# Optimization experiments

Measured on AMD Instinct MI355X. Metric: run time of the kernel, lower is better.

Reference implementation:

```python
import jax, jax.numpy as jnp
import numpy as np

B, T, IN, OUT = 32, 2048, 1024, 256
DT = 1.0
TAU_MIN, TAU_MAX = 15.0, 25.0


def setup_inputs() -> dict:
    key = jax.random.key(0)
    k1, k2, k3 = jax.random.split(key, 3)
    inputs = jax.random.normal(k1, (B, T, IN), dtype=jnp.float32)
    bound = float(np.sqrt(1.0 / IN))
    weight = jax.random.uniform(k2, (OUT, IN), minval=-bound, maxval=bound, dtype=jnp.float32)
    bias = jnp.zeros((OUT,), dtype=jnp.float32)
    tau = jax.random.uniform(k3, (OUT,), minval=TAU_MIN, maxval=TAU_MAX, dtype=jnp.float32)
    decay = jnp.exp(-DT / tau)  # per-channel leak alpha in (0,1)
    return {"inputs": inputs, "weight": weight, "bias": bias, "decay": decay}


def reference(inputs, weight, bias, decay):
    # Dense projection: [B,T,IN] @ [IN,OUT] -> [B,T,OUT]
    current = jnp.einsum("bti,oi->bto", inputs, weight) + bias
    # Leaky integrator: u_t = alpha * u_{t-1} + (1-alpha) * x_t, u_0 = 0
    one_minus = 1.0 - decay

    def step(u, x):  # u,x: [B,OUT]
        u = decay * u + one_minus * x
        return u, u

    u0 = jnp.zeros((inputs.shape[0], weight.shape[0]), dtype=current.dtype)
    _, us = jax.lax.scan(step, u0, jnp.swapaxes(current, 0, 1))  # [T,B,OUT]
    return jnp.swapaxes(us, 0, 1)  # [B,T,OUT]
```

## Files before the change

kernel.cpp:

```cpp
#include <hip/hip_runtime.h>

#define B_   32
#define T_   2048
#define IN_  1024
#define OUT_ 256
#define M_   (B_ * T_)

#define BM 128
#define BN 256
#define BK 64
#define NSTEPS (IN_ / BK)
#define THREADS 512

#define NC 16
#define LC (T_ / NC)

typedef __attribute__((ext_vector_type(4))) float f32x4;
typedef __attribute__((ext_vector_type(8))) __bf16 bf16x8;

__device__ __forceinline__ unsigned int f2bf_pk(float a, float b) {
    unsigned int ua = __float_as_uint(a);
    unsigned int ub = __float_as_uint(b);
    ua = (ua + 0x7fffu + ((ua >> 16) & 1u)) >> 16;
    ub = (ub + 0x7fffu + ((ub >> 16) & 1u)) >> 16;
    return ua | (ub << 16);
}

__global__ __launch_bounds__(256) void convert_w(const float* __restrict__ W,
                                                 unsigned short* __restrict__ Wb) {
    const int i = blockIdx.x * 256 + threadIdx.x;
    const float4 v = ((const float4*)W)[i];
    uint2 o;
    o.x = f2bf_pk(v.x, v.y);
    o.y = f2bf_pk(v.z, v.w);
    ((uint2*)Wb)[i] = o;
}

__global__ __launch_bounds__(THREADS, 1) void gemm_mfma(
    const float* __restrict__ A, const unsigned short* __restrict__ Wb,
    const float* __restrict__ bias, float* __restrict__ C) {
    __shared__ __align__(16) unsigned short Abuf[2][BM * BK];
    __shared__ __align__(16) unsigned short Bbuf[2][BN * BK];

    const int tid  = threadIdx.x;
    const int lane = tid & 63;
    const int wid  = tid >> 6;
    const int wm   = wid >> 2;
    const int wn   = wid & 3;
    const int l15  = lane & 15;
    const int l4   = lane >> 4;
    const int bm0  = blockIdx.x * BM;

    const int gA = tid & 7;
    int rA[2], ldsA[2];
    const float* gsrcA[2];
#pragma unroll
    for (int i = 0; i < 2; ++i) {
        const int q = tid + i * THREADS;
        rA[i] = q >> 3;
        ldsA[i] = rA[i] * BK + ((gA ^ (rA[i] & 7)) << 3);
        gsrcA[i] = A + (size_t)(bm0 + rA[i]) * IN_ + gA * 8;
    }
    int ldsB[4];
    const unsigned short* gsrcB[4];
#pragma unroll
    for (int i = 0; i < 4; ++i) {
        const int q = tid + i * THREADS;
        const int r = q >> 3;
        ldsB[i] = r * BK + ((gA ^ (r & 7)) << 3);
        gsrcB[i] = Wb + (size_t)r * IN_ + gA * 8;
    }

    f32x4 acc[4][4] = {};
    float4 a0[2], a1[2];
    int4 bst[4];

#pragma unroll
    for (int i = 0; i < 2; ++i) {
        a0[i] = *(const float4*)(gsrcA[i]);
        a1[i] = *(const float4*)(gsrcA[i] + 4);
    }
#pragma unroll
    for (int i = 0; i < 4; ++i) bst[i] = *(const int4*)(gsrcB[i]);
#pragma unroll
    for (int i = 0; i < 2; ++i) {
        int4 w;
        w.x = f2bf_pk(a0[i].x, a0[i].y); w.y = f2bf_pk(a0[i].z, a0[i].w);
        w.z = f2bf_pk(a1[i].x, a1[i].y); w.w = f2bf_pk(a1[i].z, a1[i].w);
        *(int4*)&Abuf[0][ldsA[i]] = w;
    }
#pragma unroll
    for (int i = 0; i < 4; ++i) *(int4*)&Bbuf[0][ldsB[i]] = bst[i];
    __syncthreads();

    int cur = 0;
    for (int step = 0; step < NSTEPS; ++step) {
        const int nxt = step + 1;
        if (nxt < NSTEPS) {
            const int k0 = nxt * BK;
#pragma unroll
            for (int i = 0; i < 2; ++i) {
                a0[i] = *(const float4*)(gsrcA[i] + k0);
                a1[i] = *(const float4*)(gsrcA[i] + k0 + 4);
            }
#pragma unroll
            for (int i = 0; i < 4; ++i) bst[i] = *(const int4*)(gsrcB[i] + k0);
        }
#pragma unroll
        for (int ks = 0; ks < 2; ++ks) {
            bf16x8 af[4], bfv[4];
            const int kg = (ks << 2) + l4;
#pragma unroll
            for (int mi = 0; mi < 4; ++mi) {
                const int row = wm * 64 + mi * 16 + l15;
                af[mi] = *(const bf16x8*)&Abuf[cur][row * BK + ((kg ^ (row & 7)) << 3)];
            }
#pragma unroll
            for (int ni = 0; ni < 4; ++ni) {
                const int col = wn * 64 + ni * 16 + l15;
                bfv[ni] = *(const bf16x8*)&Bbuf[cur][col * BK + ((kg ^ (col & 7)) << 3)];
            }
#pragma unroll
            for (int mi = 0; mi < 4; ++mi)
#pragma unroll
                for (int ni = 0; ni < 4; ++ni)
                    acc[mi][ni] = __builtin_amdgcn_mfma_f32_16x16x32_bf16(
                        af[mi], bfv[ni], acc[mi][ni], 0, 0, 0);
        }
        if (nxt < NSTEPS) {
#pragma unroll
            for (int i = 0; i < 2; ++i) {
                int4 w;
                w.x = f2bf_pk(a0[i].x, a0[i].y); w.y = f2bf_pk(a0[i].z, a0[i].w);
                w.z = f2bf_pk(a1[i].x, a1[i].y); w.w = f2bf_pk(a1[i].z, a1[i].w);
                *(int4*)&Abuf[cur ^ 1][ldsA[i]] = w;
            }
#pragma unroll
            for (int i = 0; i < 4; ++i) *(int4*)&Bbuf[cur ^ 1][ldsB[i]] = bst[i];
        }
        __syncthreads();
        cur ^= 1;
    }

#pragma unroll
    for (int ni = 0; ni < 4; ++ni) {
        const int col = wn * 64 + ni * 16 + l15;
        const float bv = bias[col];
#pragma unroll
        for (int mi = 0; mi < 4; ++mi) {
            const int row0 = bm0 + wm * 64 + mi * 16 + (l4 << 2);
#pragma unroll
            for (int r = 0; r < 4; ++r)
                C[(size_t)(row0 + r) * OUT_ + col] = acc[mi][ni][r] + bv;
        }
    }
}

__global__ __launch_bounds__(256) void gemm_bias(const float* __restrict__ A,
                                                 const float* __restrict__ W,
                                                 const float* __restrict__ bias,
                                                 float* __restrict__ C) {
    __shared__ float As[16][64 + 4];
    __shared__ float Ws[16][64 + 4];
    const int bm = blockIdx.y * 64;
    const int bn = blockIdx.x * 64;
    const int tid = threadIdx.x;
    const int tx = tid & 15, ty = tid >> 4;
    const int lr = tid >> 2, lc = (tid & 3) << 2;
    float acc[4][4] = {};
    const float* Ap = A + (size_t)(bm + lr) * IN_ + lc;
    const float* Wp = W + (size_t)(bn + lr) * IN_ + lc;
    for (int k0 = 0; k0 < IN_; k0 += 16) {
        const float4 a = *(const float4*)(Ap + k0);
        const float4 w = *(const float4*)(Wp + k0);
        __syncthreads();
        As[lc + 0][lr] = a.x; As[lc + 1][lr] = a.y; As[lc + 2][lr] = a.z; As[lc + 3][lr] = a.w;
        Ws[lc + 0][lr] = w.x; Ws[lc + 1][lr] = w.y; Ws[lc + 2][lr] = w.z; Ws[lc + 3][lr] = w.w;
        __syncthreads();
#pragma unroll
        for (int kk = 0; kk < 16; ++kk) {
            const float4 av = *(const float4*)&As[kk][ty << 2];
            const float4 wv = *(const float4*)&Ws[kk][tx << 2];
            const float a0[4] = {av.x, av.y, av.z, av.w};
            const float w0[4] = {wv.x, wv.y, wv.z, wv.w};
#pragma unroll
            for (int i = 0; i < 4; ++i)
#pragma unroll
                for (int j = 0; j < 4; ++j) acc[i][j] = fmaf(a0[i], w0[j], acc[i][j]);
        }
    }
#pragma unroll
    for (int i = 0; i < 4; ++i) {
        const size_t row = (size_t)(bm + (ty << 2) + i);
#pragma unroll
        for (int j = 0; j < 4; ++j)
            C[row * OUT_ + bn + (tx << 2) + j] = acc[i][j] + bias[bn + (tx << 2) + j];
    }
}

__global__ __launch_bounds__(OUT_) void scan_pass1(const float* __restrict__ C,
                                                   const float* __restrict__ decay,
                                                   float* __restrict__ chunkend) {
    const int b = blockIdx.x / NC;
    const int c = blockIdx.x % NC;
    const int o = threadIdx.x;
    const float alpha = decay[o];
    const float om = 1.0f - alpha;
    const float* p = C + ((size_t)b * T_ + (size_t)c * LC) * OUT_ + o;
    float u = 0.0f;
#pragma unroll 4
    for (int t = 0; t < LC; ++t) u = fmaf(alpha, u, om * p[(size_t)t * OUT_]);
    chunkend[((size_t)b * NC + c) * OUT_ + o] = u;
}

__global__ __launch_bounds__(OUT_) void scan_pass2(const float* __restrict__ chunkend,
                                                   const float* __restrict__ decay,
                                                   float* __restrict__ carryin) {
    const int b = blockIdx.x;
    const int o = threadIdx.x;
    const float alpha = decay[o];
    const float aL = powf(alpha, (float)LC);
    float carry = 0.0f;
    for (int c = 0; c < NC; ++c) {
        const size_t idx = ((size_t)b * NC + c) * OUT_ + o;
        carryin[idx] = carry;
        carry = fmaf(aL, carry, chunkend[idx]);
    }
}

__global__ __launch_bounds__(OUT_) void scan_pass3(float* __restrict__ C,
                                                   const float* __restrict__ decay,
                                                   const float* __restrict__ carryin) {
    const int b = blockIdx.x / NC;
    const int c = blockIdx.x % NC;
    const int o = threadIdx.x;
    const float alpha = decay[o];
    const float om = 1.0f - alpha;
    float u = carryin[((size_t)b * NC + c) * OUT_ + o];
    float* p = C + ((size_t)b * T_ + (size_t)c * LC) * OUT_ + o;
#pragma unroll 4
    for (int t = 0; t < LC; ++t) {
        const float x = p[(size_t)t * OUT_];
        u = fmaf(alpha, u, om * x);
        p[(size_t)t * OUT_] = u;
    }
}

__global__ __launch_bounds__(OUT_) void scan_simple(float* __restrict__ C,
                                                    const float* __restrict__ decay) {
    const int b = blockIdx.x;
    const int o = threadIdx.x;
    const float alpha = decay[o];
    const float om = 1.0f - alpha;
    float u = 0.0f;
    float* p = C + (size_t)b * T_ * OUT_ + o;
    for (int t = 0; t < T_; ++t) {
        const float x = p[(size_t)t * OUT_];
        u = fmaf(alpha, u, om * x);
        p[(size_t)t * OUT_] = u;
    }
}

extern "C" void kernel_launch(void* const* d_in, const int* in_sizes, int n_in,
                              void* d_out, int out_size, void* d_ws, size_t ws_size,
                              hipStream_t stream) {
    const float* inputs = (const float*)d_in[0];
    const float* weight = (const float*)d_in[1];
    const float* bias   = (const float*)d_in[2];
    const float* decay  = (const float*)d_in[3];
    float* out = (float*)d_out;

    const size_t wbytes = (size_t)OUT_ * IN_ * 2;
    const size_t sbytes = (size_t)2 * B_ * NC * OUT_ * 4;

    if (ws_size >= wbytes + sbytes) {
        unsigned short* Wb = (unsigned short*)d_ws;
        float* chunkend = (float*)((char*)d_ws + wbytes);
        float* carryin  = chunkend + (size_t)B_ * NC * OUT_;

        convert_w<<<(OUT_ * IN_ / 4) / 256, 256, 0, stream>>>(weight, Wb);
        gemm_mfma<<<M_ / BM, THREADS, 0, stream>>>(inputs, Wb, bias, out);
        scan_pass1<<<B_ * NC, OUT_, 0, stream>>>(out, decay, chunkend);
        scan_pass2<<<B_, OUT_, 0, stream>>>(chunkend, decay, carryin);
        scan_pass3<<<B_ * NC, OUT_, 0, stream>>>(out, decay, carryin);
    } else {
        dim3 g(OUT_ / 64, M_ / 64);
        gemm_bias<<<g, 256, 0, stream>>>(inputs, weight, bias, out);
        scan_simple<<<B_, OUT_, 0, stream>>>(out, decay);
    }
}
```

Baseline: 136.0 us.

## Fuse chunk-scan pass into GEMM epilogue and store bf16 intermediate

The GEMM epilogue now writes the projected tile (bias added) to shared memory as bf16, stores it to a bf16 workspace, and computes per-chunk scan end values directly from LDS with 32-step chunks. The carry pass and a vectorized final scan kernel then read the bf16 intermediate instead of re-reading the fp32 output twice. This removes a full fp32 read pass and halves intermediate traffic, at the cost of bf16 rounding of the pre-scan current and a longer sequential carry pass over 64 chunks per batch.

```diff
diff --git a/kernel.cpp b/kernel.cpp
--- a/kernel.cpp
+++ b/kernel.cpp
@@ -12,8 +12,9 @@
 #define NSTEPS (IN_ / BK)
 #define THREADS 512
 
-#define NC 16
-#define LC (T_ / NC)
+#define LC 32
+#define NC (T_ / LC)
+#define XPAD 264
 
 typedef __attribute__((ext_vector_type(4))) float f32x4;
 typedef __attribute__((ext_vector_type(8))) __bf16 bf16x8;
@@ -24,6 +25,13 @@
     ua = (ua + 0x7fffu + ((ua >> 16) & 1u)) >> 16;
     ub = (ub + 0x7fffu + ((ub >> 16) & 1u)) >> 16;
     return ua | (ub << 16);
+}
+__device__ __forceinline__ unsigned short f2bf1(float a) {
+    unsigned int ua = __float_as_uint(a);
+    return (unsigned short)((ua + 0x7fffu + ((ua >> 16) & 1u)) >> 16);
+}
+__device__ __forceinline__ float bf2f(unsigned short s) {
+    return __uint_as_float((unsigned int)s << 16);
 }
 
 __global__ __launch_bounds__(256) void convert_w(const float* __restrict__ W,
@@ -36,11 +44,13 @@
     ((uint2*)Wb)[i] = o;
 }
 
-__global__ __launch_bounds__(THREADS, 1) void gemm_mfma(
+__global__ __launch_bounds__(THREADS, 1) void gemm_fused(
     const float* __restrict__ A, const unsigned short* __restrict__ Wb,
-    const float* __restrict__ bias, float* __restrict__ C) {
-    __shared__ __align__(16) unsigned short Abuf[2][BM * BK];
-    __shared__ __align__(16) unsigned short Bbuf[2][BN * BK];
+    const float* __restrict__ bias, const float* __restrict__ decay,
+    unsigned short* __restrict__ Xb, float* __restrict__ chunkend) {
+    __shared__ __align__(16) char smem[98304];
+#define ABUF(c) ((unsigned short*)(smem + (c) * 16384))
+#define BBUF(c) ((unsigned short*)(smem + 32768 + (c) * 32768))
 
     const int tid  = threadIdx.x;
     const int lane = tid & 63;
@@ -87,10 +97,10 @@
         int4 w;
         w.x = f2bf_pk(a0[i].x, a0[i].y); w.y = f2bf_pk(a0[i].z, a0[i].w);
         w.z = f2bf_pk(a1[i].x, a1[i].y); w.w = f2bf_pk(a1[i].z, a1[i].w);
-        *(int4*)&Abuf[0][ldsA[i]] = w;
-    }
-#pragma unroll
-    for (int i = 0; i < 4; ++i) *(int4*)&Bbuf[0][ldsB[i]] = bst[i];
+        *(int4*)&ABUF(0)[ldsA[i]] = w;
+    }
+#pragma unroll
+    for (int i = 0; i < 4; ++i) *(int4*)&BBUF(0)[ldsB[i]] = bst[i];
     __syncthreads();
 
     int cur = 0;
@@ -113,12 +123,12 @@
 #pragma unroll
             for (int mi = 0; mi < 4; ++mi) {
                 const int row = wm * 64 + mi * 16 + l15;
-                af[mi] = *(const bf16x8*)&Abuf[cur][row * BK + ((kg ^ (row & 7)) << 3)];
+                af[mi] = *(const bf16x8*)&ABUF(cur)[row * BK + ((kg ^ (row & 7)) << 3)];
             }
 #pragma unroll
             for (int ni = 0; ni < 4; ++ni) {
                 const int col = wn * 64 + ni * 16 + l15;
-                bfv[ni] = *(const bf16x8*)&Bbuf[cur][col * BK + ((kg ^ (col & 7)) << 3)];
+                bfv[ni] = *(const bf16x8*)&BBUF(cur)[col * BK + ((kg ^ (col & 7)) << 3)];
             }
 #pragma unroll
             for (int mi = 0; mi < 4; ++mi)
@@ -133,26 +143,100 @@
                 int4 w;
                 w.x = f2bf_pk(a0[i].x, a0[i].y); w.y = f2bf_pk(a0[i].z, a0[i].w);
                 w.z = f2bf_pk(a1[i].x, a1[i].y); w.w = f2bf_pk(a1[i].z, a1[i].w);
-                *(int4*)&Abuf[cur ^ 1][ldsA[i]] = w;
+                *(int4*)&ABUF(cur ^ 1)[ldsA[i]] = w;
             }
 #pragma unroll
-            for (int i = 0; i < 4; ++i) *(int4*)&Bbuf[cur ^ 1][ldsB[i]] = bst[i];
+            for (int i = 0; i < 4; ++i) *(int4*)&BBUF(cur ^ 1)[ldsB[i]] = bst[i];
         }
         __syncthreads();
         cur ^= 1;
     }
 
+    unsigned short* xt = (unsigned short*)smem;
 #pragma unroll
     for (int ni = 0; ni < 4; ++ni) {
         const int col = wn * 64 + ni * 16 + l15;
         const float bv = bias[col];
 #pragma unroll
         for (int mi = 0; mi < 4; ++mi) {
-            const int row0 = bm0 + wm * 64 + mi * 16 + (l4 << 2);
+            const int r0 = wm * 64 + mi * 16 + (l4 << 2);
 #pragma unroll
             for (int r = 0; r < 4; ++r)
-                C[(size_t)(row0 + r) * OUT_ + col] = acc[mi][ni][r] + bv;
-        }
+                xt[(r0 + r) * XPAD + col] = f2bf1(acc[mi][ni][r] + bv);
+        }
+    }
+    __syncthreads();
+
+    const int b  = bm0 >> 11;
+    const int c0 = (bm0 >> 5) & 63;
+
+    {
+        const int cr = tid >> 5;
+        const int cg = (tid & 31) << 3;
+#pragma unroll
+        for (int it = 0; it < 8; ++it) {
+            const int row = it * 16 + cr;
+            bf16x8 v = *(const bf16x8*)&xt[row * XPAD + cg];
+            *(bf16x8*)&Xb[(size_t)(bm0 + row) * OUT_ + cg] = v;
+        }
+    }
+
+    for (int task = tid; task < 4 * OUT_; task += THREADS) {
+        const int cl  = task >> 8;
+        const int col = task & 255;
+        const float alpha = decay[col];
+        const float om = 1.0f - alpha;
+        float u = 0.0f;
+        const unsigned short* p = &xt[(cl * LC) * XPAD + col];
+#pragma unroll
+        for (int t = 0; t < LC; ++t)
+            u = fmaf(alpha, u, om * bf2f(p[t * XPAD]));
+        chunkend[(size_t)(b * NC + c0 + cl) * OUT_ + col] = u;
+    }
+#undef ABUF
+#undef BBUF
+}
+
+__global__ __launch_bounds__(OUT_) void carry_pass(const float* __restrict__ chunkend,
+                                                   const float* __restrict__ decay,
+                                                   float* __restrict__ carryin) {
+    const int b = blockIdx.x;
+    const int o = threadIdx.x;
+    const float alpha = decay[o];
+    float aL = alpha;
+#pragma unroll
+    for (int i = 1; i < LC; ++i) aL *= alpha;
+    float carry = 0.0f;
+    for (int c = 0; c < NC; ++c) {
+        const size_t idx = (size_t)(b * NC + c) * OUT_ + o;
+        carryin[idx] = carry;
+        carry = fmaf(aL, carry, chunkend[idx]);
+    }
+}
+
+__global__ __launch_bounds__(256) void scan_final(const unsigned short* __restrict__ Xb,
+                                                  const float* __restrict__ decay,
+                                                  const float* __restrict__ carryin,
+                                                  float* __restrict__ out) {
+    const int unit = blockIdx.x * 4 + (threadIdx.x >> 6);
+    const int l    = threadIdx.x & 63;
+    const int col  = l << 2;
+    const int b    = unit >> 6;
+    const int c    = unit & 63;
+
+    const float4 al = *(const float4*)&decay[col];
+    const float4 om = {1.0f - al.x, 1.0f - al.y, 1.0f - al.z, 1.0f - al.w};
+    float4 u = *(const float4*)&carryin[(size_t)unit * OUT_ + col];
+
+    const size_t base = (size_t)(b * T_ + c * LC) * OUT_ + col;
+#pragma unroll 4
+    for (int t = 0; t < LC; ++t) {
+        const ushort4 xv = *(const ushort4*)&Xb[base + (size_t)t * OUT_];
+        u.x = fmaf(al.x, u.x, om.x * bf2f(xv.x));
+        u.y = fmaf(al.y, u.y, om.y * bf2f(xv.y));
+        u.z = fmaf(al.z, u.z, om.z * bf2f(xv.z));
+        u.w = fmaf(al.w, u.w, om.w * bf2f(xv.w));
+        *(float4*)&out[base + (size_t)t * OUT_] = u;
     }
 }
 
@@ -198,54 +282,6 @@
     }
 }
 
-__global__ __launch_bounds__(OUT_) void scan_pass1(const float* __restrict__ C,
-                                                   const float* __restrict__ decay,
-                                                   float* __restrict__ chunkend) {
-    const int b = blockIdx.x / NC;
-    const int c = blockIdx.x % NC;
-    const int o = threadIdx.x;
-    const float alpha = decay[o];
-    const float om = 1.0f - alpha;
-    const float* p = C + ((size_t)b * T_ + (size_t)c * LC) * OUT_ + o;
-    float u = 0.0f;
-#pragma unroll 4
-    for (int t = 0; t < LC; ++t) u = fmaf(alpha, u, om * p[(size_t)t * OUT_]);
-    chunkend[((size_t)b * NC + c) * OUT_ + o] = u;
-}
-
-__global__ __launch_bounds__(OUT_) void scan_pass2(const float* __restrict__ chunkend,
-                                                   const float* __restrict__ decay,
-                                                   float* __restrict__ carryin) {
-    const int b = blockIdx.x;
-    const int o = threadIdx.x;
-    const float alpha = decay[o];
-    const float aL = powf(alpha, (float)LC);
-    float carry = 0.0f;
-    for (int c = 0; c < NC; ++c) {
-        const size_t idx = ((size_t)b * NC + c) * OUT_ + o;
-        carryin[idx] = carry;
-        carry = fmaf(aL, carry, chunkend[idx]);
-    }
-}
-
-__global__ __launch_bounds__(OUT_) void scan_pass3(float* __restrict__ C,
-                                                   const float* __restrict__ decay,
-                                                   const float* __restrict__ carryin) {
-    const int b = blockIdx.x / NC;
-    const int c = blockIdx.x % NC;
-    const int o = threadIdx.x;
-    const float alpha = decay[o];
-    const float om = 1.0f - alpha;
-    float u = carryin[((size_t)b * NC + c) * OUT_ + o];
-    float* p = C + ((size_t)b * T_ + (size_t)c * LC) * OUT_ + o;
-#pragma unroll 4
-    for (int t = 0; t < LC; ++t) {
-        const float x = p[(size_t)t * OUT_];
-        u = fmaf(alpha, u, om * x);
-        p[(size_t)t * OUT_] = u;
-    }
-}
-
 __global__ __launch_bounds__(OUT_) void scan_simple(float* __restrict__ C,
                                                     const float* __restrict__ decay) {
     const int b = blockIdx.x;
@@ -270,19 +306,23 @@
     const float* decay  = (const float*)d_in[3];
     float* out = (float*)d_out;
 
-    const size_t wbytes = (size_t)OUT_ * IN_ * 2;
-    const size_t sbytes = (size_t)2 * B_ * NC * OUT_ * 4;
-
-    if (ws_size >= wbytes + sbytes) {
-        unsigned short* Wb = (unsigned short*)d_ws;
-        float* chunkend = (float*)((char*)d_ws + wbytes);
-        float* carryin  = chunkend + (size_t)B_ * NC * OUT_;
+    const size_t wb_bytes = (size_t)OUT_ * IN_ * 2;
+    const size_t ce_bytes = (size_t)B_ * NC * OUT_ * 4;
+    const size_t ci_bytes = ce_bytes;
+    const size_t x_bytes  = (size_t)M_ * OUT_ * 2;
+    const size_t need = wb_bytes + ce_bytes + ci_bytes + x_bytes;
+
+    if (ws_size >= need) {
+        char* w = (char*)d_ws;
+        unsigned short* Wb = (unsigned short*)w;
+        float* chunkend    = (float*)(w + wb_bytes);
+        float* carryin     = (float*)(w + wb_bytes + ce_bytes);
+        unsigned short* Xb = (unsigned short*)(w + wb_bytes + ce_bytes + ci_bytes);
 
         convert_w<<<(OUT_ * IN_ / 4) / 256, 256, 0, stream>>>(weight, Wb);
-        gemm_mfma<<<M_ / BM, THREADS, 0, stream>>>(inputs, Wb, bias, out);
-        scan_pass1<<<B_ * NC, OUT_, 0, stream>>>(out, decay, chunkend);
-        scan_pass2<<<B_, OUT_, 0, stream>>>(chunkend, decay, carryin);
-        scan_pass3<<<B_ * NC, OUT_, 0, stream>>>(out, decay, carryin);
+        gemm_fused<<<M_ / BM, THREADS, 0, stream>>>(inputs, Wb, bias, decay, Xb, chunkend);
+        carry_pass<<<B_, OUT_, 0, stream>>>(chunkend, decay, carryin);
+        scan_final<<<(B_ * NC) / 4, 256, 0, stream>>>(Xb, decay, carryin, out);
     } else {
         dim3 g(OUT_ / 64, M_ / 64);
         gemm_bias<<<g, 256, 0, stream>>>(inputs, weight, bias, out);
```

Result: faster. 121.1 us (-10.9%).
